# Optimization experiments

Hardware: AMD Instinct MI355X
Metric: run time of the kernel (lower is better)

The kernel has to match this reference:

```python
import jax, jax.numpy as jnp
import numpy as np

B, L = 16384, 1024
BIAS = (1, 1)


def setup_inputs() -> dict:
    key = jax.random.key(0)
    k1, k2 = jax.random.split(key)
    c = jax.random.normal(k1, (B, L), dtype=jnp.float32)
    y = jax.random.randint(k2, (B, L), 0, 2, dtype=jnp.int32)
    return {"c": c, "y": y}


def reference(c, y):
    # BPMLL loss. The double sum over (k,l) in Y_i x Ybar_i of exp(c_l - c_k)
    # factors exactly: (sum_k y_k exp(-c_k)) * (sum_l ybar_l exp(c_l)).
    y_f = y.astype(jnp.float32)          # [B, L]
    y_bar = 1.0 - y_f                    # [B, L]
    y_norm = jnp.sum(y_f, axis=1) ** BIAS[0]        # [B]
    y_bar_norm = jnp.sum(y_bar, axis=1) ** BIAS[1]  # [B]
    pos_term = jnp.sum(y_f * jnp.exp(-c), axis=1)   # sum_k y_k exp(-c_k)
    neg_term = jnp.sum(y_bar * jnp.exp(c), axis=1)  # sum_l ybar_l exp(c_l)
    loss = (pos_term * neg_term) / (y_norm * y_bar_norm)  # [B]
    return jnp.mean(loss)  # reduction='mean' -> scalar
```

## Files before the change

### kernel.cpp

```cpp
#include <hip/hip_runtime.h>


#define NROWS 16384
#define NCOLS 1024
#define WPB 4
#define NBLOCKS 2048

__device__ __forceinline__ void elem(float cv, int yv,
                                     float& pos, float& neg, float& cnt) {
    float t = __expf(yv ? -cv : cv);
    pos += yv ? t : 0.f;
    neg += yv ? 0.f : t;
    cnt += (float)yv;
}

__device__ __forceinline__ void consume4(const float4& cv, const int4& yv,
                                         float& pos, float& neg, float& cnt) {
    elem(cv.x, yv.x, pos, neg, cnt);
    elem(cv.y, yv.y, pos, neg, cnt);
    elem(cv.z, yv.z, pos, neg, cnt);
    elem(cv.w, yv.w, pos, neg, cnt);
}

__device__ __forceinline__ float row_finish(float pos, float neg, float cnt) {
#pragma unroll
    for (int off = 1; off < 64; off <<= 1) {
        pos += __shfl_xor(pos, off);
        neg += __shfl_xor(neg, off);
        cnt += __shfl_xor(cnt, off);
    }
    return (pos * neg) / (cnt * ((float)NCOLS - cnt));
}

__global__ __launch_bounds__(256, 4) void bpmll_rows_kernel(
    const float* __restrict__ c, const int* __restrict__ y,
    float* __restrict__ partials) {
    const int wave = threadIdx.x >> 6;
    const int lane = threadIdx.x & 63;
    const int row0 = (blockIdx.x * WPB + wave) * 2;

    const float4* __restrict__ cA = (const float4*)(c + (size_t)row0 * NCOLS);
    const float4* __restrict__ cB = cA + NCOLS / 4;
    const int4* __restrict__ yA = (const int4*)(y + (size_t)row0 * NCOLS);
    const int4* __restrict__ yB = yA + NCOLS / 4;

    float4 ca[4], cb[4];
    int4 ya[4], yb[4];
#pragma unroll
    for (int i = 0; i < 4; ++i) ca[i] = cA[lane + 64 * i];
#pragma unroll
    for (int i = 0; i < 4; ++i) ya[i] = yA[lane + 64 * i];
#pragma unroll
    for (int i = 0; i < 4; ++i) cb[i] = cB[lane + 64 * i];
#pragma unroll
    for (int i = 0; i < 4; ++i) yb[i] = yB[lane + 64 * i];

    __builtin_amdgcn_sched_barrier(0);

    float posA = 0.f, negA = 0.f, cntA = 0.f;
#pragma unroll
    for (int i = 0; i < 4; ++i) consume4(ca[i], ya[i], posA, negA, cntA);
    float lossA = row_finish(posA, negA, cntA);

    float posB = 0.f, negB = 0.f, cntB = 0.f;
#pragma unroll
    for (int i = 0; i < 4; ++i) consume4(cb[i], yb[i], posB, negB, cntB);
    float lossB = row_finish(posB, negB, cntB);

    __shared__ float acc[WPB];
    if (lane == 0) acc[wave] = lossA + lossB;
    __syncthreads();
    if (threadIdx.x == 0) {
        partials[blockIdx.x] =
            (acc[0] + acc[1] + acc[2] + acc[3]) * (1.0f / (float)NROWS);
    }
}

__global__ __launch_bounds__(256) void bpmll_reduce_kernel(
    const float* __restrict__ partials, float* __restrict__ out) {
    float4 v0 = ((const float4*)partials)[threadIdx.x];
    float4 v1 = ((const float4*)partials)[threadIdx.x + 256];
    float s = (v0.x + v0.y + v0.z + v0.w) + (v1.x + v1.y + v1.z + v1.w);
#pragma unroll
    for (int off = 1; off < 64; off <<= 1) s += __shfl_xor(s, off);

    __shared__ float smem[4];
    const int lane = threadIdx.x & 63;
    const int wave = threadIdx.x >> 6;
    if (lane == 0) smem[wave] = s;
    __syncthreads();
    if (threadIdx.x == 0) out[0] = smem[0] + smem[1] + smem[2] + smem[3];
}

extern "C" void kernel_launch(void* const* d_in, const int* in_sizes, int n_in,
                              void* d_out, int out_size, void* d_ws, size_t ws_size,
                              hipStream_t stream) {
    const float* c = (const float*)d_in[0];
    const int* y = (const int*)d_in[1];
    float* partials = (float*)d_ws;
    float* out = (float*)d_out;

    bpmll_rows_kernel<<<NBLOCKS, 256, 0, stream>>>(c, y, partials);
    bpmll_reduce_kernel<<<1, 256, 0, stream>>>(partials, out);
}
```

Baseline: 144.1 us.

## Process eight rows per wave with double-buffered nontemporal loads

Cuts the grid from 2048 to 512 blocks so each wave handles eight rows instead of two. The next row's c and y data are prefetched into a second register buffer while the current row is reduced. Loads now use nontemporal hints, and the reduce kernel reads 512 scalar partials instead of vectors. Fewer waves in flight lowers memory-level parallelism on a bandwidth-bound stream, and that may not be made up by the software prefetch.

```diff
diff --git a/kernel.cpp b/kernel.cpp
--- a/kernel.cpp
+++ b/kernel.cpp
@@ -4,7 +4,11 @@
 #define NROWS 16384
 #define NCOLS 1024
 #define WPB 4
-#define NBLOCKS 2048
+#define NBLOCKS 512
+#define ROWS_PER_WAVE (NROWS / (NBLOCKS * WPB))
+
+typedef float vf4 __attribute__((ext_vector_type(4)));
+typedef int vi4 __attribute__((ext_vector_type(4)));
 
 __device__ __forceinline__ void elem(float cv, int yv,
                                      float& pos, float& neg, float& cnt) {
@@ -14,7 +18,7 @@
     cnt += (float)yv;
 }
 
-__device__ __forceinline__ void consume4(const float4& cv, const int4& yv,
+__device__ __forceinline__ void consume4(const vf4& cv, const vi4& yv,
                                          float& pos, float& neg, float& cnt) {
     elem(cv.x, yv.x, pos, neg, cnt);
     elem(cv.y, yv.y, pos, neg, cnt);
@@ -32,43 +36,50 @@
     return (pos * neg) / (cnt * ((float)NCOLS - cnt));
 }
 
-__global__ __launch_bounds__(256, 4) void bpmll_rows_kernel(
+__global__ __launch_bounds__(256, 2) void bpmll_rows_kernel(
     const float* __restrict__ c, const int* __restrict__ y,
     float* __restrict__ partials) {
     const int wave = threadIdx.x >> 6;
     const int lane = threadIdx.x & 63;
-    const int row0 = (blockIdx.x * WPB + wave) * 2;
+    const int gw = blockIdx.x * WPB + wave;
+    const int row0 = gw * ROWS_PER_WAVE;
 
-    const float4* __restrict__ cA = (const float4*)(c + (size_t)row0 * NCOLS);
-    const float4* __restrict__ cB = cA + NCOLS / 4;
-    const int4* __restrict__ yA = (const int4*)(y + (size_t)row0 * NCOLS);
-    const int4* __restrict__ yB = yA + NCOLS / 4;
+    const vf4* __restrict__ cp = (const vf4*)(c + (size_t)row0 * NCOLS);
+    const vi4* __restrict__ yp = (const vi4*)(y + (size_t)row0 * NCOLS);
 
-    float4 ca[4], cb[4];
-    int4 ya[4], yb[4];
+    vf4 cbuf[2][4];
+    vi4 ybuf[2][4];
+
 #pragma unroll
-    for (int i = 0; i < 4; ++i) ca[i] = cA[lane + 64 * i];
+    for (int i = 0; i < 4; ++i)
+        cbuf[0][i] = __builtin_nontemporal_load(&cp[lane + 64 * i]);
 #pragma unroll
-    for (int i = 0; i < 4; ++i) ya[i] = yA[lane + 64 * i];
+    for (int i = 0; i < 4; ++i)
+        ybuf[0][i] = __builtin_nontemporal_load(&yp[lane + 64 * i]);
+
+    float wave_loss = 0.f;
 #pragma unroll
-    for (int i = 0; i < 4; ++i) cb[i] = cB[lane + 64 * i];
+    for (int r = 0; r < ROWS_PER_WAVE; ++r) {
+        const int cur = r & 1, nxt = cur ^ 1;
+        if (r < ROWS_PER_WAVE - 1) {
+            const vf4* cn = cp + (size_t)(r + 1) * (NCOLS / 4);
+            const vi4* yn = yp + (size_t)(r + 1) * (NCOLS / 4);
 #pragma unroll
-    for (int i = 0; i < 4; ++i) yb[i] = yB[lane + 64 * i];
-
-    __builtin_amdgcn_sched_barrier(0);
-
-    float posA = 0.f, negA = 0.f, cntA = 0.f;
+            for (int i = 0; i < 4; ++i)
+                cbuf[nxt][i] = __builtin_nontemporal_load(&cn[lane + 64 * i]);
 #pragma unroll
-    for (int i = 0; i < 4; ++i) consume4(ca[i], ya[i], posA, negA, cntA);
-    float lossA = row_finish(posA, negA, cntA);
-
-    float posB = 0.f, negB = 0.f, cntB = 0.f;
+            for (int i = 0; i < 4; ++i)
+                ybuf[nxt][i] = __builtin_nontemporal_load(&yn[lane + 64 * i]);
+        }
+        float pos = 0.f, neg = 0.f, cnt = 0.f;
 #pragma unroll
-    for (int i = 0; i < 4; ++i) consume4(cb[i], yb[i], posB, negB, cntB);
-    float lossB = row_finish(posB, negB, cntB);
+        for (int i = 0; i < 4; ++i)
+            consume4(cbuf[cur][i], ybuf[cur][i], pos, neg, cnt);
+        wave_loss += row_finish(pos, neg, cnt);
+    }
 
     __shared__ float acc[WPB];
-    if (lane == 0) acc[wave] = lossA + lossB;
+    if (lane == 0) acc[wave] = wave_loss;
     __syncthreads();
     if (threadIdx.x == 0) {
         partials[blockIdx.x] =
@@ -78,9 +89,7 @@
 
 __global__ __launch_bounds__(256) void bpmll_reduce_kernel(
     const float* __restrict__ partials, float* __restrict__ out) {
-    float4 v0 = ((const float4*)partials)[threadIdx.x];
-    float4 v1 = ((const float4*)partials)[threadIdx.x + 256];
-    float s = (v0.x + v0.y + v0.z + v0.w) + (v1.x + v1.y + v1.z + v1.w);
+    float s = partials[threadIdx.x] + partials[threadIdx.x + 256];
 #pragma unroll
     for (int off = 1; off < 64; off <<= 1) s += __shfl_xor(s, off);
 
```

Measured after the change: 137.3 us, median of 2. -4.7%, faster.
